# Optimization experiments

Measured on AMD Instinct MI355X. Metric: run time of the kernel, lower is better.

The kernel has to match this reference:

```python
import jax, jax.numpy as jnp
import numpy as np

N_NODES = 81
N_EDGES = 1620
IN_DIM = 10
HIDDEN = 8192
ACTIONS = 729


def setup_inputs() -> dict:
    key = jax.random.key(0)
    ks = jax.random.split(key, 8)
    x = jax.random.normal(ks[0], (N_NODES, IN_DIM), dtype=jnp.float32)
    edge_index = jax.random.randint(ks[1], (2, N_EDGES), 0, N_NODES, dtype=jnp.int64)
    W_gcn = jax.random.normal(ks[2], (IN_DIM, HIDDEN), dtype=jnp.float32) / np.sqrt(IN_DIM)
    b_gcn = jnp.zeros((HIDDEN,), dtype=jnp.float32)
    ln_g = jnp.ones((HIDDEN,), dtype=jnp.float32)
    ln_b = jnp.zeros((HIDDEN,), dtype=jnp.float32)
    W1 = jax.random.normal(ks[3], (HIDDEN, HIDDEN), dtype=jnp.float32) / np.sqrt(HIDDEN)
    b1 = jnp.zeros((HIDDEN,), dtype=jnp.float32)
    W2 = jax.random.normal(ks[4], (HIDDEN, ACTIONS), dtype=jnp.float32) / np.sqrt(HIDDEN)
    b2 = jnp.zeros((ACTIONS,), dtype=jnp.float32)
    return {"x": x, "edge_index": edge_index, "W_gcn": W_gcn, "b_gcn": b_gcn,
            "ln_g": ln_g, "ln_b": ln_b, "W1": W1, "b1": b1, "W2": W2, "b2": b2}


def _gcn_conv(x, edge_index, W, b):
    # GCNConv with added self-loops and symmetric D^-1/2 (A+I) D^-1/2 normalization
    n = x.shape[0]
    loops = jnp.arange(n, dtype=edge_index.dtype)
    src = jnp.concatenate([edge_index[0], loops])  # [E+N]
    dst = jnp.concatenate([edge_index[1], loops])
    h = x @ W  # [N, H] — transform before propagate, as in PyG
    deg = jnp.zeros((n,), dtype=h.dtype).at[dst].add(1.0)
    dinv = jnp.where(deg > 0, jax.lax.rsqrt(deg), 0.0)
    norm = dinv[src] * dinv[dst]  # [E+N]
    msg = h[src] * norm[:, None]
    out = jnp.zeros_like(h).at[dst].add(msg)
    return out + b


def _layer_norm(h, g, b, eps=1e-5):
    mu = jnp.mean(h, axis=-1, keepdims=True)
    var = jnp.mean(jnp.square(h - mu), axis=-1, keepdims=True)
    return (h - mu) * jax.lax.rsqrt(var + eps) * g + b


def reference(x, edge_index, W_gcn, b_gcn, ln_g, ln_b, W1, b1, W2, b2):
    h = jax.nn.relu(_gcn_conv(x, edge_index, W_gcn, b_gcn))  # [81, H]
    h = _layer_norm(h, ln_g, ln_b)
    # global_add_pool with batch = zeros(81): sum all nodes into one graph row
    g = jnp.sum(h, axis=0, keepdims=True)  # [1, H]
    g = jax.nn.relu(g @ W1 + b1)
    logits = g @ W2 + b2  # [1, ACTIONS]
    return jax.nn.log_softmax(logits, axis=1)
```

## Files before the change

### kernel.cpp

```cpp
#include <hip/hip_runtime.h>
#include <math.h>

#define N_NODES 81
#define N_EDGES 1620
#define IN_DIM 10
#define HIDDEN 8192
#define ACTIONS 729

__global__ __launch_bounds__(256) void stats_kernel(const float* __restrict__ x,
                                                    const int* __restrict__ ei,
                                                    const float* __restrict__ Wg,
                                                    const float* __restrict__ bg,
                                                    float* __restrict__ yr_all,
                                                    float* __restrict__ stats,
                                                    float* __restrict__ logits) {
    const int n = blockIdx.x;
    const int t = threadIdx.x;
    __shared__ float deg[N_NODES];
    __shared__ float yr[IN_DIM];
    __shared__ float red[8];

    if (t < N_NODES) deg[t] = 1.0f;
    if (t < IN_DIM) yr[t] = 0.0f;
    __syncthreads();
    for (int e = t; e < N_EDGES; e += 256) atomicAdd(&deg[ei[N_EDGES + e]], 1.0f);
    __syncthreads();
    if (t < N_NODES) deg[t] = rsqrtf(deg[t]);
    __syncthreads();
    const float dn = deg[n];
    for (int e = t; e < N_EDGES; e += 256) {
        if (ei[N_EDGES + e] == n) {
            int s = ei[e];
            float nrm = deg[s] * dn;
            #pragma unroll
            for (int c = 0; c < IN_DIM; ++c) atomicAdd(&yr[c], nrm * x[s * IN_DIM + c]);
        }
    }
    if (t == 0) {
        float nrm = dn * dn;
        #pragma unroll
        for (int c = 0; c < IN_DIM; ++c) atomicAdd(&yr[c], nrm * x[n * IN_DIM + c]);
    }
    __syncthreads();
    if (t < IN_DIM) yr_all[n * IN_DIM + t] = yr[t];
    if (n == 0) for (int a = t; a < ACTIONS; a += 256) logits[a] = 0.f;

    const float4* Wg4 = (const float4*)Wg;
    const float4* bg4 = (const float4*)bg;
    float s = 0.f, s2 = 0.f;
    #pragma unroll
    for (int k = 0; k < 8; ++k) {
        int j4 = t + k * 256;
        float4 h = bg4[j4];
        #pragma unroll
        for (int c = 0; c < IN_DIM; ++c) {
            float4 w = Wg4[c * (HIDDEN / 4) + j4];
            float yc = yr[c];
            h.x = fmaf(yc, w.x, h.x);
            h.y = fmaf(yc, w.y, h.y);
            h.z = fmaf(yc, w.z, h.z);
            h.w = fmaf(yc, w.w, h.w);
        }
        h.x = fmaxf(h.x, 0.f); h.y = fmaxf(h.y, 0.f);
        h.z = fmaxf(h.z, 0.f); h.w = fmaxf(h.w, 0.f);
        s  += h.x + h.y + h.z + h.w;
        s2 += h.x * h.x + h.y * h.y + h.z * h.z + h.w * h.w;
    }
    #pragma unroll
    for (int off = 32; off > 0; off >>= 1) { s += __shfl_xor(s, off); s2 += __shfl_xor(s2, off); }
    int wave = t >> 6, lane = t & 63;
    if (lane == 0) { red[wave] = s; red[4 + wave] = s2; }
    __syncthreads();
    if (t == 0) {
        float S  = red[0] + red[1] + red[2] + red[3];
        float S2 = red[4] + red[5] + red[6] + red[7];
        float mu = S * (1.f / HIDDEN);
        float var = S2 * (1.f / HIDDEN) - mu * mu;
        stats[2 * n]     = mu;
        stats[2 * n + 1] = rsqrtf(var + 1e-5f);
    }
}

__global__ __launch_bounds__(256) void gemv1_kernel(const float* __restrict__ Wg,
                                                    const float* __restrict__ bg,
                                                    const float* __restrict__ lng,
                                                    const float* __restrict__ lnb,
                                                    const float* __restrict__ yr_all,
                                                    const float* __restrict__ stats,
                                                    const float* __restrict__ W1,
                                                    float* __restrict__ partial) {
    const int ct = blockIdx.x;
    const int ch = blockIdx.y;
    const int row0 = ch * 64;
    const int t = threadIdx.x;

    __shared__ float syr[N_NODES * IN_DIM];
    __shared__ float sstat[2 * N_NODES];
    __shared__ float sw[IN_DIM][64];
    __shared__ float gred[4][64];
    __shared__ float gl[64];

    for (int i = t; i < N_NODES * IN_DIM; i += 256) syr[i] = yr_all[i];
    for (int i = t; i < 2 * N_NODES; i += 256) sstat[i] = stats[i];
    if (t < 64) {
        #pragma unroll
        for (int c = 0; c < IN_DIM; ++c) sw[c][t] = Wg[c * HIDDEN + row0 + t];
    }
    __syncthreads();

    {
        const int r = t & 63, grp = t >> 6;
        const float bgv = bg[row0 + r];
        float acc = 0.f;
        for (int n = grp; n < N_NODES; n += 4) {
            float h = bgv;
            #pragma unroll
            for (int c = 0; c < IN_DIM; ++c) h = fmaf(syr[n * IN_DIM + c], sw[c][r], h);
            h = fmaxf(h, 0.f);
            acc += (h - sstat[2 * n]) * sstat[2 * n + 1];
        }
        gred[grp][r] = acc;
    }
    __syncthreads();
    if (t < 64)
        gl[t] = (gred[0][t] + gred[1][t] + gred[2][t] + gred[3][t]) * lng[row0 + t]
                + (float)N_NODES * lnb[row0 + t];
    __syncthreads();

    float4 acc = make_float4(0.f, 0.f, 0.f, 0.f);
    const float* p = W1 + (size_t)row0 * HIDDEN + ct * 1024 + t * 4;
    #pragma unroll 8
    for (int i = 0; i < 64; ++i) {
        const float* q = p + (size_t)i * HIDDEN;
        float4 w;
        w.x = __builtin_nontemporal_load(q);
        w.y = __builtin_nontemporal_load(q + 1);
        w.z = __builtin_nontemporal_load(q + 2);
        w.w = __builtin_nontemporal_load(q + 3);
        float gi = gl[i];
        acc.x = fmaf(gi, w.x, acc.x);
        acc.y = fmaf(gi, w.y, acc.y);
        acc.z = fmaf(gi, w.z, acc.z);
        acc.w = fmaf(gi, w.w, acc.w);
    }
    ((float4*)(partial + (size_t)ch * HIDDEN + ct * 1024))[t] = acc;
}

__global__ __launch_bounds__(256) void gemv2_kernel(const float* __restrict__ partial,
                                                    const float* __restrict__ b1,
                                                    const float* __restrict__ W2,
                                                    float* __restrict__ logits) {
    const int ch = blockIdx.x;
    const int row0 = ch * 32;
    const int t = threadIdx.x;
    __shared__ float sred[8][32];
    __shared__ float gl[32];

    {
        const int r = t & 31, grp = t >> 5;
        float a = 0.f;
        #pragma unroll 4
        for (int c = grp; c < 128; c += 8) a += partial[(size_t)c * HIDDEN + row0 + r];
        sred[grp][r] = a;
    }
    __syncthreads();
    if (t < 32) {
        float S = b1[row0 + t];
        #pragma unroll
        for (int gq = 0; gq < 8; ++gq) S += sred[gq][t];
        gl[t] = fmaxf(S, 0.f);
    }
    __syncthreads();

    float s0 = 0.f, s1 = 0.f, s2v = 0.f;
    const bool has2 = (t + 512) < ACTIONS;
    #pragma unroll 4
    for (int i = 0; i < 32; ++i) {
        float gi = gl[i];
        const float* r = W2 + (size_t)(row0 + i) * ACTIONS;
        s0 = fmaf(gi, r[t], s0);
        s1 = fmaf(gi, r[t + 256], s1);
        if (has2) s2v = fmaf(gi, r[t + 512], s2v);
    }
    atomicAdd(&logits[t], s0);
    atomicAdd(&logits[t + 256], s1);
    if (has2) atomicAdd(&logits[t + 512], s2v);
}

__global__ __launch_bounds__(256) void logsoftmax_kernel(const float* __restrict__ logits,
                                                         const float* __restrict__ b2,
                                                         float* __restrict__ out) {
    __shared__ float red[4];
    const int t = threadIdx.x;
    const bool has2 = (t + 512) < ACTIONS;
    float l0 = logits[t] + b2[t];
    float l1 = logits[t + 256] + b2[t + 256];
    float l2 = has2 ? (logits[t + 512] + b2[t + 512]) : -INFINITY;
    float m = fmaxf(fmaxf(l0, l1), l2);
    #pragma unroll
    for (int off = 32; off > 0; off >>= 1) m = fmaxf(m, __shfl_xor(m, off));
    int wave = t >> 6, lane = t & 63;
    if (lane == 0) red[wave] = m;
    __syncthreads();
    float M = fmaxf(fmaxf(red[0], red[1]), fmaxf(red[2], red[3]));
    __syncthreads();
    float e = __expf(l0 - M) + __expf(l1 - M) + (has2 ? __expf(l2 - M) : 0.f);
    #pragma unroll
    for (int off = 32; off > 0; off >>= 1) e += __shfl_xor(e, off);
    if (lane == 0) red[wave] = e;
    __syncthreads();
    float S = red[0] + red[1] + red[2] + red[3];
    float L = logf(S);
    out[t] = l0 - M - L;
    out[t + 256] = l1 - M - L;
    if (has2) out[t + 512] = l2 - M - L;
}

extern "C" void kernel_launch(void* const* d_in, const int* in_sizes, int n_in,
                              void* d_out, int out_size, void* d_ws, size_t ws_size,
                              hipStream_t stream) {
    const float* x    = (const float*)d_in[0];
    const int*   ei   = (const int*)  d_in[1];
    const float* Wg   = (const float*)d_in[2];
    const float* bg   = (const float*)d_in[3];
    const float* lng  = (const float*)d_in[4];
    const float* lnb  = (const float*)d_in[5];
    const float* W1   = (const float*)d_in[6];
    const float* b1   = (const float*)d_in[7];
    const float* W2   = (const float*)d_in[8];
    const float* b2   = (const float*)d_in[9];
    float* out = (float*)d_out;

    float* ws = (float*)d_ws;
    float* logits  = ws;
    float* stats   = ws + 1024;
    float* yr_all  = ws + 1280;
    float* partial = ws + 4096;

    stats_kernel<<<N_NODES, 256, 0, stream>>>(x, ei, Wg, bg, yr_all, stats, logits);
    gemv1_kernel<<<dim3(8, 128), 256, 0, stream>>>(Wg, bg, lng, lnb, yr_all, stats, W1, partial);
    gemv2_kernel<<<256, 256, 0, stream>>>(partial, b1, W2, logits);
    logsoftmax_kernel<<<1, 256, 0, stream>>>(logits, b2, out);
}
```

Measured before the change: 97.92 us.

## Fuse log-softmax into gemv2 via last-block counter; use plain float4 W1 loads

Drops the separate single-block log-softmax launch. The gemv2 blocks now increment a global counter after their logit atomics, and the last block to arrive computes the log-softmax in place. This removes one kernel launch and its gap, at the cost of one atomic per block and a memory-ordering dependence on the waitcnt plus relaxed atomic loads. The gemv1 W1 stream also switches from four scalar nontemporal loads to a single vectorized float4 load, which changes the cache hint.

Result: faster. 95.17 us (-2.8%).

```diff
diff --git a/kernel.cpp b/kernel.cpp
--- a/kernel.cpp
+++ b/kernel.cpp
@@ -13,7 +13,8 @@
                                                     const float* __restrict__ bg,
                                                     float* __restrict__ yr_all,
                                                     float* __restrict__ stats,
-                                                    float* __restrict__ logits) {
+                                                    float* __restrict__ logits,
+                                                    unsigned* __restrict__ counter) {
     const int n = blockIdx.x;
     const int t = threadIdx.x;
     __shared__ float deg[N_NODES];
@@ -43,7 +44,10 @@
     }
     __syncthreads();
     if (t < IN_DIM) yr_all[n * IN_DIM + t] = yr[t];
-    if (n == 0) for (int a = t; a < ACTIONS; a += 256) logits[a] = 0.f;
+    if (n == 0) {
+        for (int a = t; a < ACTIONS; a += 256) logits[a] = 0.f;
+        if (t == 0) *counter = 0u;
+    }
 
     const float4* Wg4 = (const float4*)Wg;
     const float4* bg4 = (const float4*)bg;
@@ -128,15 +132,10 @@
     __syncthreads();
 
     float4 acc = make_float4(0.f, 0.f, 0.f, 0.f);
-    const float* p = W1 + (size_t)row0 * HIDDEN + ct * 1024 + t * 4;
+    const float4* p = (const float4*)(W1 + (size_t)row0 * HIDDEN + ct * 1024) + t;
     #pragma unroll 8
     for (int i = 0; i < 64; ++i) {
-        const float* q = p + (size_t)i * HIDDEN;
-        float4 w;
-        w.x = __builtin_nontemporal_load(q);
-        w.y = __builtin_nontemporal_load(q + 1);
-        w.z = __builtin_nontemporal_load(q + 2);
-        w.w = __builtin_nontemporal_load(q + 3);
+        float4 w = p[(size_t)i * (HIDDEN / 4)];
         float gi = gl[i];
         acc.x = fmaf(gi, w.x, acc.x);
         acc.y = fmaf(gi, w.y, acc.y);
@@ -146,15 +145,19 @@
     ((float4*)(partial + (size_t)ch * HIDDEN + ct * 1024))[t] = acc;
 }
 
-__global__ __launch_bounds__(256) void gemv2_kernel(const float* __restrict__ partial,
-                                                    const float* __restrict__ b1,
-                                                    const float* __restrict__ W2,
-                                                    float* __restrict__ logits) {
+__global__ __launch_bounds__(256) void gemv2_lsm_kernel(const float* __restrict__ partial,
+                                                        const float* __restrict__ b1,
+                                                        const float* __restrict__ W2,
+                                                        const float* __restrict__ b2,
+                                                        float* __restrict__ logits,
+                                                        unsigned* __restrict__ counter,
+                                                        float* __restrict__ out) {
     const int ch = blockIdx.x;
     const int row0 = ch * 32;
     const int t = threadIdx.x;
     __shared__ float sred[8][32];
     __shared__ float gl[32];
+    __shared__ int isLast;
 
     {
         const int r = t & 31, grp = t >> 5;
@@ -185,35 +188,38 @@
     atomicAdd(&logits[t], s0);
     atomicAdd(&logits[t + 256], s1);
     if (has2) atomicAdd(&logits[t + 512], s2v);
-}
-
-__global__ __launch_bounds__(256) void logsoftmax_kernel(const float* __restrict__ logits,
-                                                         const float* __restrict__ b2,
-                                                         float* __restrict__ out) {
-    __shared__ float red[4];
-    const int t = threadIdx.x;
-    const bool has2 = (t + 512) < ACTIONS;
-    float l0 = logits[t] + b2[t];
-    float l1 = logits[t + 256] + b2[t + 256];
-    float l2 = has2 ? (logits[t + 512] + b2[t + 512]) : -INFINITY;
-    float m = fmaxf(fmaxf(l0, l1), l2);
-    #pragma unroll
-    for (int off = 32; off > 0; off >>= 1) m = fmaxf(m, __shfl_xor(m, off));
-    int wave = t >> 6, lane = t & 63;
-    if (lane == 0) red[wave] = m;
-    __syncthreads();
-    float M = fmaxf(fmaxf(red[0], red[1]), fmaxf(red[2], red[3]));
-    __syncthreads();
-    float e = __expf(l0 - M) + __expf(l1 - M) + (has2 ? __expf(l2 - M) : 0.f);
-    #pragma unroll
-    for (int off = 32; off > 0; off >>= 1) e += __shfl_xor(e, off);
-    if (lane == 0) red[wave] = e;
-    __syncthreads();
-    float S = red[0] + red[1] + red[2] + red[3];
-    float L = logf(S);
-    out[t] = l0 - M - L;
-    out[t + 256] = l1 - M - L;
-    if (has2) out[t + 512] = l2 - M - L;
+
+    asm volatile("s_waitcnt vmcnt(0)" ::: "memory");
+    __syncthreads();
+    if (t == 0) isLast = (atomicAdd(counter, 1u) == 255u) ? 1 : 0;
+    __syncthreads();
+
+    if (isLast) {
+        float l0 = __hip_atomic_load(&logits[t], __ATOMIC_RELAXED,
+                                     __HIP_MEMORY_SCOPE_AGENT) + b2[t];
+        float l1 = __hip_atomic_load(&logits[t + 256], __ATOMIC_RELAXED,
+                                     __HIP_MEMORY_SCOPE_AGENT) + b2[t + 256];
+        float l2 = has2 ? (__hip_atomic_load(&logits[t + 512], __ATOMIC_RELAXED,
+                                             __HIP_MEMORY_SCOPE_AGENT) + b2[t + 512])
+                        : -INFINITY;
+        float m = fmaxf(fmaxf(l0, l1), l2);
+        #pragma unroll
+        for (int off = 32; off > 0; off >>= 1) m = fmaxf(m, __shfl_xor(m, off));
+        if ((t & 63) == 0) sred[0][t >> 6] = m;
+        __syncthreads();
+        float M = fmaxf(fmaxf(sred[0][0], sred[0][1]), fmaxf(sred[0][2], sred[0][3]));
+        __syncthreads();
+        float e = __expf(l0 - M) + __expf(l1 - M) + (has2 ? __expf(l2 - M) : 0.f);
+        #pragma unroll
+        for (int off = 32; off > 0; off >>= 1) e += __shfl_xor(e, off);
+        if ((t & 63) == 0) sred[0][t >> 6] = e;
+        __syncthreads();
+        float Se = sred[0][0] + sred[0][1] + sred[0][2] + sred[0][3];
+        float L = logf(Se);
+        out[t] = l0 - M - L;
+        out[t + 256] = l1 - M - L;
+        if (has2) out[t + 512] = l2 - M - L;
+    }
 }
 
 extern "C" void kernel_launch(void* const* d_in, const int* in_sizes, int n_in,
@@ -232,13 +238,13 @@
     float* out = (float*)d_out;
 
     float* ws = (float*)d_ws;
-    float* logits  = ws;
-    float* stats   = ws + 1024;
+    float* logits    = ws;
+    unsigned* counter = (unsigned*)(ws + 1024);
+    float* stats   = ws + 1088;
     float* yr_all  = ws + 1280;
     float* partial = ws + 4096;
 
-    stats_kernel<<<N_NODES, 256, 0, stream>>>(x, ei, Wg, bg, yr_all, stats, logits);
+    stats_kernel<<<N_NODES, 256, 0, stream>>>(x, ei, Wg, bg, yr_all, stats, logits, counter);
     gemv1_kernel<<<dim3(8, 128), 256, 0, stream>>>(Wg, bg, lng, lnb, yr_all, stats, W1, partial);
-    gemv2_kernel<<<256, 256, 0, stream>>>(partial, b1, W2, logits);
-    logsoftmax_kernel<<<1, 256, 0, stream>>>(logits, b2, out);
-}
+    gemv2_lsm_kernel<<<256, 256, 0, stream>>>(partial, b1, W2, b2, logits, counter, out);
+}
```
